# Performance work log

Hardware: AMD Instinct MI355X
Metric: run time of the kernel (lower is better)

## Reference

```python
import jax, jax.numpy as jnp
import numpy as np

N_NODES = 50000


def mean_aggregate(x, src, dst):
    # gather source features, scatter-sum to destinations, divide by in-degree
    msgs = x[src]                                             # [E, D]
    summed = jax.ops.segment_sum(msgs, dst, num_segments=N_NODES)  # [N, D]
    deg = jax.ops.segment_sum(jnp.ones_like(dst, dtype=x.dtype), dst,
                              num_segments=N_NODES)           # [N]
    return summed / jnp.clip(deg, 1.0)[:, None]


def sage_conv(x, src, dst, Wl, Wr, b):
    # PyG SAGEConv (aggr='mean'): lin_l(agg) + lin_r(x); bias only on lin_l
    agg = mean_aggregate(x, src, dst)
    return agg @ Wl + b + x @ Wr


def setup_inputs() -> dict:
    key = jax.random.key(0)
    ks = jax.random.split(key, 8)
    x = jax.random.normal(ks[0], (N_NODES, 64), dtype=jnp.float32)
    edge_index = jax.random.randint(ks[1], (2, 800000), 0, N_NODES, dtype=jnp.int32)
    W1l = jax.random.normal(ks[2], (64, 128), dtype=jnp.float32) * (1.0 / np.sqrt(64))
    W1r = jax.random.normal(ks[3], (64, 128), dtype=jnp.float32) * (1.0 / np.sqrt(64))
    b1 = jnp.zeros((128,), dtype=jnp.float32)
    W2l = jax.random.normal(ks[4], (128, 40), dtype=jnp.float32) * (1.0 / np.sqrt(128))
    W2r = jax.random.normal(ks[5], (128, 40), dtype=jnp.float32) * (1.0 / np.sqrt(128))
    b2 = jnp.zeros((40,), dtype=jnp.float32)
    return {"x": x, "edge_index": edge_index, "W1l": W1l, "W1r": W1r, "b1": b1,
            "W2l": W2l, "W2r": W2r, "b2": b2}


def reference(x, edge_index, W1l, W1r, b1, W2l, W2r, b2):
    src, dst = edge_index[0], edge_index[1]
    h = sage_conv(x, src, dst, W1l, W1r, b1)
    h = jax.nn.relu(h)
    # dropout p=0.5 is identity in eval mode (self.training=False)
    h = sage_conv(h, src, dst, W2l, W2r, b2)
    return h, jax.nn.log_softmax(h, axis=1)
```

## Files before the change

kernel.cpp:

```cpp
#include <hip/hip_runtime.h>
#include <hip/hip_bf16.h>
#include <math.h>

#define N_NODES 50000
#define N_EDGES 800000
#define D0 64
#define D1 128
#define D2 40

#define NB  256
#define NPB 196

typedef short s16x8 __attribute__((ext_vector_type(8)));
typedef float f32x4 __attribute__((ext_vector_type(4)));

static __device__ __forceinline__ unsigned short f2bf(float v) {
    __hip_bfloat16 hb = __float2bfloat16(v);
    return *(unsigned short*)&hb;
}

__global__ __launch_bounds__(256) void bucket_count_kernel(
        const int* __restrict__ dst, int* __restrict__ bcount, int E) {
    __shared__ int h[NB];
    int t = threadIdx.x;
    h[t] = 0;
    __syncthreads();
    int e0 = blockIdx.x * 2048;
    for (int i = t; i < 2048; i += 256) {
        int e = e0 + i;
        if (e < E) atomicAdd(&h[(unsigned)dst[e] / NPB], 1);
    }
    __syncthreads();
    if (h[t]) atomicAdd(&bcount[t], h[t]);
}

__global__ void bucket_scan_kernel(const int* __restrict__ bcount,
                                   int* __restrict__ bbase, int* __restrict__ bcursor) {
    __shared__ int sd[NB];
    int t = threadIdx.x;
    int v = bcount[t];
    sd[t] = v;
    __syncthreads();
    for (int off = 1; off < NB; off <<= 1) {
        int u = (t >= off) ? sd[t - off] : 0;
        __syncthreads();
        sd[t] += u;
        __syncthreads();
    }
    int ex = sd[t] - v;
    bbase[t] = ex;
    bcursor[t] = ex;
}

__global__ __launch_bounds__(256) void bucket_scatter_kernel(
        const int* __restrict__ src, const int* __restrict__ dst,
        int* __restrict__ bcursor, unsigned* __restrict__ ebuf, int E) {
    __shared__ int h[NB];
    __shared__ int base[NB];
    int t = threadIdx.x;
    int e0 = blockIdx.x * 4096;
    h[t] = 0;
    __syncthreads();
    for (int i = t; i < 4096; i += 256) {
        int e = e0 + i;
        if (e < E) atomicAdd(&h[(unsigned)dst[e] / NPB], 1);
    }
    __syncthreads();
    if (h[t] > 0) base[t] = atomicAdd(&bcursor[t], h[t]);
    h[t] = 0;
    __syncthreads();
    for (int i = t; i < 4096; i += 256) {
        int e = e0 + i;
        if (e < E) {
            unsigned d = (unsigned)dst[e];
            unsigned b = d / NPB;
            unsigned ld = d - b * NPB;
            int k = atomicAdd(&h[b], 1);
            ebuf[base[b] + k] = (ld << 17) | (unsigned)src[e];
        }
    }
}

__global__ __launch_bounds__(256) void bucket_fill_kernel(
        const unsigned* __restrict__ ebuf, const int* __restrict__ bbase,
        int* __restrict__ rowptr, int* __restrict__ csr, int E, int N) {
    __shared__ int cnt[256];
    __shared__ int sd[256];
    int b = blockIdx.x, t = threadIdx.x;
    int s0 = bbase[b];
    int s1 = (b < NB - 1) ? bbase[b + 1] : E;
    int lo = b * NPB;
    cnt[t] = 0;
    __syncthreads();
    for (int i = s0 + t; i < s1; i += 256)
        atomicAdd(&cnt[ebuf[i] >> 17], 1);
    __syncthreads();
    int v = cnt[t];
    sd[t] = v;
    __syncthreads();
    for (int off = 1; off < 256; off <<= 1) {
        int u = (t >= off) ? sd[t - off] : 0;
        __syncthreads();
        sd[t] += u;
        __syncthreads();
    }
    int ex = sd[t] - v;
    int node = lo + t;
    if (t < NPB && node < N) rowptr[node] = s0 + ex;
    cnt[t] = s0 + ex;
    __syncthreads();
    for (int i = s0 + t; i < s1; i += 256) {
        unsigned pk = ebuf[i];
        int p = atomicAdd(&cnt[pk >> 17], 1);
        csr[p] = (int)(pk & 0x1FFFFu);
    }
    if (b == NB - 1 && t == 0) rowptr[N] = E;
}


__global__ void cast_x_kernel(const float* __restrict__ x, unsigned short* __restrict__ xh, int n) {
    int i = (blockIdx.x * blockDim.x + threadIdx.x) * 4;
    if (i < n) {
        float4 v = *(const float4*)(x + i);
        xh[i + 0] = f2bf(v.x);
        xh[i + 1] = f2bf(v.y);
        xh[i + 2] = f2bf(v.z);
        xh[i + 3] = f2bf(v.w);
    }
}


__global__ void pack_w1_kernel(const float* __restrict__ W1l, const float* __restrict__ W1r,
                               unsigned short* __restrict__ Wpk) {
    int f = blockIdx.x;
    int lane = threadIdx.x;
    int nt = f & 7;
    int col = nt * 16 + (lane & 15);
    int kbase = (f >> 3) * 32 + (lane >> 4) * 8;
    unsigned short* o = Wpk + ((size_t)f * 64 + lane) * 8;
#pragma unroll
    for (int j = 0; j < 8; ++j) {
        int k = kbase + j;
        float w = (k < 64) ? W1r[k * 128 + col] : W1l[(k - 64) * 128 + col];
        o[j] = f2bf(w);
    }
}

__global__ void pack_w2_kernel(const float* __restrict__ W2l, const float* __restrict__ W2r,
                               unsigned short* __restrict__ Wpk) {
    int f = blockIdx.x;
    int lane = threadIdx.x;
    int nt = f % 5;
    int col = nt * 16 + (lane & 15);
    int kbase = (f / 5) * 32 + (lane >> 4) * 8;
    unsigned short* o = Wpk + ((size_t)f * 64 + lane) * 8;
#pragma unroll
    for (int j = 0; j < 8; ++j) {
        int k = kbase + j;
        float w = (col < 40) ? W2l[k * 40 + col] : W2r[k * 40 + (col - 40)];
        o[j] = f2bf(w);
    }
}


__global__ void agg1_kernel(const unsigned short* __restrict__ xh, const int* __restrict__ rowptr,
                            const int* __restrict__ csr, unsigned short* __restrict__ aggh, int N) {
    int wid = (blockIdx.x * blockDim.x + threadIdx.x) >> 6;
    int lane = threadIdx.x & 63;
    if (wid >= N) return;
    int beg = rowptr[wid], end = rowptr[wid + 1];
    int deg = end - beg;
    int l = lane & 7, g = lane >> 3;
    float acc[8];
#pragma unroll
    for (int k = 0; k < 8; ++k) acc[k] = 0.f;
    int jmax = (deg + 7) >> 3;
    for (int j = 0; j < jmax; j += 2) {
        int s[2]; float w[2];
#pragma unroll
        for (int u = 0; u < 2; ++u) {
            int slot = (j + u) * 8 + g;
            int e = beg + slot;
            e = (e < end) ? e : (end - 1);
            s[u] = csr[e];
            w[u] = (slot < deg) ? 1.f : 0.f;
        }
#pragma unroll
        for (int u = 0; u < 2; ++u) {
            uint4 v = *(const uint4*)(xh + (size_t)s[u] * D0 + l * 8);
            float f0 = __uint_as_float(v.x << 16), f1 = __uint_as_float(v.x & 0xffff0000u);
            float f2 = __uint_as_float(v.y << 16), f3 = __uint_as_float(v.y & 0xffff0000u);
            float f4 = __uint_as_float(v.z << 16), f5 = __uint_as_float(v.z & 0xffff0000u);
            float f6 = __uint_as_float(v.w << 16), f7 = __uint_as_float(v.w & 0xffff0000u);
            acc[0] = fmaf(w[u], f0, acc[0]); acc[1] = fmaf(w[u], f1, acc[1]);
            acc[2] = fmaf(w[u], f2, acc[2]); acc[3] = fmaf(w[u], f3, acc[3]);
            acc[4] = fmaf(w[u], f4, acc[4]); acc[5] = fmaf(w[u], f5, acc[5]);
            acc[6] = fmaf(w[u], f6, acc[6]); acc[7] = fmaf(w[u], f7, acc[7]);
        }
    }
#pragma unroll
    for (int off = 8; off <= 32; off <<= 1) {
#pragma unroll
        for (int k = 0; k < 8; ++k) acc[k] += __shfl_xor(acc[k], off);
    }
    float inv = 1.f / (float)max(deg, 1);
    if (g == 0) {
        unsigned o0 = (unsigned)f2bf(acc[0] * inv) | ((unsigned)f2bf(acc[1] * inv) << 16);
        unsigned o1 = (unsigned)f2bf(acc[2] * inv) | ((unsigned)f2bf(acc[3] * inv) << 16);
        unsigned o2 = (unsigned)f2bf(acc[4] * inv) | ((unsigned)f2bf(acc[5] * inv) << 16);
        unsigned o3 = (unsigned)f2bf(acc[6] * inv) | ((unsigned)f2bf(acc[7] * inv) << 16);
        uint4 pk; pk.x = o0; pk.y = o1; pk.z = o2; pk.w = o3;
        *(uint4*)(aggh + (size_t)wid * D0 + l * 8) = pk;
    }
}


__global__ void agg2_kernel(const float* __restrict__ p2, const float* __restrict__ r2,
                            const int* __restrict__ rowptr, const int* __restrict__ csr,
                            float* __restrict__ out, float* __restrict__ out2, int N) {
    int wid = (blockIdx.x * blockDim.x + threadIdx.x) >> 6;
    int lane = threadIdx.x & 63;
    if (wid >= N) return;
    int beg = rowptr[wid], end = rowptr[wid + 1];
    int deg = end - beg;
    int g = lane / 10;
    int l = lane - g * 10;
    bool gv = g < 6;
    float ax = 0.f, ay = 0.f, az = 0.f, aw = 0.f;
    int jmax = (deg + 5) / 6;
    for (int j = 0; j < jmax; j += 4) {
        int s[4]; float w[4];
#pragma unroll
        for (int u = 0; u < 4; ++u) {
            int slot = (j + u) * 6 + g;
            int e = beg + slot;
            e = (e < end) ? e : (end - 1);
            s[u] = csr[e];
            w[u] = (gv && slot < deg) ? 1.f : 0.f;
        }
#pragma unroll
        for (int u = 0; u < 4; ++u) {
            float4 v = *(const float4*)(p2 + (size_t)s[u] * D2 + l * 4);
            ax = fmaf(w[u], v.x, ax); ay = fmaf(w[u], v.y, ay);
            az = fmaf(w[u], v.z, az); aw = fmaf(w[u], v.w, aw);
        }
    }
    {
        float bx = __shfl(ax, lane + 30), by = __shfl(ay, lane + 30),
              bz = __shfl(az, lane + 30), bw = __shfl(aw, lane + 30);
        if (g < 3) { ax += bx; ay += by; az += bz; aw += bw; }
        bx = __shfl(ax, lane + 20); by = __shfl(ay, lane + 20);
        bz = __shfl(az, lane + 20); bw = __shfl(aw, lane + 20);
        if (g == 0) { ax += bx; ay += by; az += bz; aw += bw; }
        bx = __shfl(ax, lane + 10); by = __shfl(ay, lane + 10);
        bz = __shfl(az, lane + 10); bw = __shfl(aw, lane + 10);
        if (g == 0) { ax += bx; ay += by; az += bz; aw += bw; }
    }
    float inv = 1.f / (float)max(deg, 1);
    bool wr = (lane < 10);
    float4 h2;
    if (wr) {
        float4 rr = *(const float4*)(r2 + (size_t)wid * D2 + lane * 4);
        h2.x = rr.x + ax * inv; h2.y = rr.y + ay * inv;
        h2.z = rr.z + az * inv; h2.w = rr.w + aw * inv;
        *(float4*)(out + (size_t)wid * D2 + lane * 4) = h2;
    }
    float m = wr ? fmaxf(fmaxf(h2.x, h2.y), fmaxf(h2.z, h2.w)) : -INFINITY;
#pragma unroll
    for (int off = 1; off < 64; off <<= 1) m = fmaxf(m, __shfl_xor(m, off));
    float s = 0.f;
    if (wr) s = expf(h2.x - m) + expf(h2.y - m) + expf(h2.z - m) + expf(h2.w - m);
#pragma unroll
    for (int off = 1; off < 64; off <<= 1) s += __shfl_xor(s, off);
    if (wr) {
        float lg = m + logf(s);
        float4 o; o.x = h2.x - lg; o.y = h2.y - lg; o.z = h2.z - lg; o.w = h2.w - lg;
        *(float4*)(out2 + (size_t)wid * D2 + lane * 4) = o;
    }
}

__global__ __launch_bounds__(256) void gemm1_mfma(
        const unsigned short* __restrict__ xh, const unsigned short* __restrict__ aggh,
        const unsigned short* __restrict__ Wpk, const float* __restrict__ b1,
        unsigned short* __restrict__ h, int N) {
    __shared__ __align__(16) unsigned short As[128 * 136];
    int t = threadIdx.x;
    int r0 = blockIdx.x * 128;
    for (int i = t; i < 2048; i += 256) {
        int r = i >> 4, c = i & 15;
        int gr = r0 + r; gr = (gr < N) ? gr : (N - 1);
        uint4 v = (c < 8) ? ((const uint4*)(xh + (size_t)gr * 64))[c]
                          : ((const uint4*)(aggh + (size_t)gr * 64))[c - 8];
        *(uint4*)(As + r * 136 + c * 8) = v;
    }
    __syncthreads();
    int w = t >> 6, lane = t & 63;
    int l15 = lane & 15, q = lane >> 4;
    f32x4 zero = {0.f, 0.f, 0.f, 0.f};
    f32x4 acc[2][8];
#pragma unroll
    for (int rt = 0; rt < 2; ++rt)
#pragma unroll
        for (int nt = 0; nt < 8; ++nt) acc[rt][nt] = zero;
    const unsigned short* abase = As + (w * 32 + l15) * 136 + q * 8;
#pragma unroll
    for (int ks = 0; ks < 4; ++ks) {
        s16x8 a0 = *(const s16x8*)(abase + ks * 32);
        s16x8 a1 = *(const s16x8*)(abase + 16 * 136 + ks * 32);
        s16x8 b[8];
#pragma unroll
        for (int nt = 0; nt < 8; ++nt)
            b[nt] = *(const s16x8*)(Wpk + ((size_t)(ks * 8 + nt) * 64 + lane) * 8);
#pragma unroll
        for (int nt = 0; nt < 8; ++nt) {
            acc[0][nt] = __builtin_amdgcn_mfma_f32_16x16x32_bf16(a0, b[nt], acc[0][nt], 0, 0, 0);
            acc[1][nt] = __builtin_amdgcn_mfma_f32_16x16x32_bf16(a1, b[nt], acc[1][nt], 0, 0, 0);
        }
    }
    int rbase = r0 + w * 32 + q * 4;
#pragma unroll
    for (int nt = 0; nt < 8; ++nt) {
        int col = nt * 16 + l15;
        float bias = b1[col];
#pragma unroll
        for (int rt = 0; rt < 2; ++rt) {
#pragma unroll
            for (int reg = 0; reg < 4; ++reg) {
                int row = rbase + rt * 16 + reg;
                if (row < N)
                    h[(size_t)row * 128 + col] = f2bf(fmaxf(acc[rt][nt][reg] + bias, 0.f));
            }
        }
    }
}

__global__ __launch_bounds__(256) void gemm2_mfma(
        const unsigned short* __restrict__ hq, const unsigned short* __restrict__ Wpk,
        const float* __restrict__ b2,
        float* __restrict__ p2, float* __restrict__ r2, int N) {
    __shared__ __align__(16) unsigned short As[128 * 136];
    int t = threadIdx.x;
    int r0 = blockIdx.x * 128;
    for (int i = t; i < 2048; i += 256) {
        int r = i >> 4, c = i & 15;
        int gr = r0 + r; gr = (gr < N) ? gr : (N - 1);
        uint4 v = ((const uint4*)(hq + (size_t)gr * 128))[c];
        *(uint4*)(As + r * 136 + c * 8) = v;
    }
    __syncthreads();
    int w = t >> 6, lane = t & 63;
    int l15 = lane & 15, q = lane >> 4;
    f32x4 zero = {0.f, 0.f, 0.f, 0.f};
    f32x4 acc[2][5];
#pragma unroll
    for (int rt = 0; rt < 2; ++rt)
#pragma unroll
        for (int nt = 0; nt < 5; ++nt) acc[rt][nt] = zero;
    const unsigned short* abase = As + (w * 32 + l15) * 136 + q * 8;
#pragma unroll
    for (int ks = 0; ks < 4; ++ks) {
        s16x8 a0 = *(const s16x8*)(abase + ks * 32);
        s16x8 a1 = *(const s16x8*)(abase + 16 * 136 + ks * 32);
        s16x8 b[5];
#pragma unroll
        for (int nt = 0; nt < 5; ++nt)
            b[nt] = *(const s16x8*)(Wpk + ((size_t)(ks * 5 + nt) * 64 + lane) * 8);
#pragma unroll
        for (int nt = 0; nt < 5; ++nt) {
            acc[0][nt] = __builtin_amdgcn_mfma_f32_16x16x32_bf16(a0, b[nt], acc[0][nt], 0, 0, 0);
            acc[1][nt] = __builtin_amdgcn_mfma_f32_16x16x32_bf16(a1, b[nt], acc[1][nt], 0, 0, 0);
        }
    }
    int rbase = r0 + w * 32 + q * 4;
#pragma unroll
    for (int nt = 0; nt < 5; ++nt) {
        int col = nt * 16 + l15;
        bool isp = col < 40;
        int oc = isp ? col : (col - 40);
        float bias = isp ? 0.f : b2[oc];
#pragma unroll
        for (int rt = 0; rt < 2; ++rt) {
#pragma unroll
            for (int reg = 0; reg < 4; ++reg) {
                int row = rbase + rt * 16 + reg;
                if (row < N) {
                    float v = acc[rt][nt][reg] + bias;
                    if (isp) p2[(size_t)row * 40 + oc] = v;
                    else     r2[(size_t)row * 40 + oc] = v;
                }
            }
        }
    }
}


extern "C" void kernel_launch(void* const* d_in, const int* in_sizes, int n_in,
                              void* d_out, int out_size, void* d_ws, size_t ws_size,
                              hipStream_t stream) {
    const float* x   = (const float*)d_in[0];
    const int*   ei  = (const int*)d_in[1];
    const float* W1l = (const float*)d_in[2];
    const float* W1r = (const float*)d_in[3];
    const float* b1  = (const float*)d_in[4];
    const float* W2l = (const float*)d_in[5];
    const float* W2r = (const float*)d_in[6];
    const float* b2  = (const float*)d_in[7];
    float* out = (float*)d_out;

    const int N = N_NODES;
    const int E = in_sizes[1] / 2;
    const int* src = ei;
    const int* dst = ei + E;

    char* p = (char*)d_ws;
    auto alloc = [&](size_t bytes) -> void* {
        void* r = (void*)p;
        p += (bytes + 255) & ~(size_t)255;
        return r;
    };
    int*      rowptr  = (int*)alloc((size_t)(N + 1) * 4);
    int*      csr     = (int*)alloc((size_t)E * 4);
    unsigned* ebuf    = (unsigned*)alloc((size_t)E * 4);
    int*      bcount  = (int*)alloc(NB * 4);
    int*      bbase   = (int*)alloc(NB * 4);
    int*      bcursor = (int*)alloc(NB * 4);
    unsigned short* xh    = (unsigned short*)alloc((size_t)N * D0 * 2);
    unsigned short* aggh  = (unsigned short*)alloc((size_t)N * D0 * 2);
    unsigned short* hbuf  = (unsigned short*)alloc((size_t)N * D1 * 2);
    unsigned short* wpk1  = (unsigned short*)alloc((size_t)32 * 64 * 8 * 2);
    unsigned short* wpk2  = (unsigned short*)alloc((size_t)20 * 64 * 8 * 2);
    float* p2buf = (float*)alloc((size_t)N * D2 * 4);
    float* r2buf = (float*)alloc((size_t)N * D2 * 4);

    hipMemsetAsync(bcount, 0, NB * 4, stream);
    bucket_count_kernel<<<(E + 2047) / 2048, 256, 0, stream>>>(dst, bcount, E);
    bucket_scan_kernel<<<1, NB, 0, stream>>>(bcount, bbase, bcursor);
    bucket_scatter_kernel<<<(E + 4095) / 4096, 256, 0, stream>>>(src, dst, bcursor, ebuf, E);
    bucket_fill_kernel<<<NB, 256, 0, stream>>>(ebuf, bbase, rowptr, csr, E, N);

    cast_x_kernel<<<(N * D0 / 4 + 255) / 256, 256, 0, stream>>>(x, xh, N * D0);
    pack_w1_kernel<<<32, 64, 0, stream>>>(W1l, W1r, wpk1);
    pack_w2_kernel<<<20, 64, 0, stream>>>(W2l, W2r, wpk2);

    agg1_kernel<<<(N * 64 + 255) / 256, 256, 0, stream>>>(xh, rowptr, csr, aggh, N);
    gemm1_mfma<<<(N + 127) / 128, 256, 0, stream>>>(xh, aggh, wpk1, b1, hbuf, N);

    gemm2_mfma<<<(N + 127) / 128, 256, 0, stream>>>(hbuf, wpk2, b2, p2buf, r2buf, N);
    agg2_kernel<<<(N * 64 + 255) / 256, 256, 0, stream>>>(p2buf, r2buf, rowptr, csr,
                                                          out, out + (size_t)N * D2, N);
}
```

Measured before the change: 202.5 us.

## Fuse prep kernels into one launch and store layer-2 messages as bf16

Merges bucket counting, the x cast and both weight-packing kernels into a single prep kernel that branches on block index. Per-block histograms replace the global atomics and the memset, and the scan kernel now sums them. The layer-2 projected messages gathered by agg2 are stored in bf16 instead of fp32, halving gather traffic at some cost in precision. Together these cut launch count and memory traffic.

```diff
diff --git a/kernel.cpp b/kernel.cpp
--- a/kernel.cpp
+++ b/kernel.cpp
@@ -19,26 +19,70 @@
     return *(unsigned short*)&hb;
 }
 
-__global__ __launch_bounds__(256) void bucket_count_kernel(
-        const int* __restrict__ dst, int* __restrict__ bcount, int E) {
-    __shared__ int h[NB];
-    int t = threadIdx.x;
-    h[t] = 0;
-    __syncthreads();
-    int e0 = blockIdx.x * 2048;
-    for (int i = t; i < 2048; i += 256) {
-        int e = e0 + i;
-        if (e < E) atomicAdd(&h[(unsigned)dst[e] / NPB], 1);
-    }
-    __syncthreads();
-    if (h[t]) atomicAdd(&bcount[t], h[t]);
-}
-
-__global__ void bucket_scan_kernel(const int* __restrict__ bcount,
+__global__ __launch_bounds__(256) void prep_kernel(
+        const float* __restrict__ x, const int* __restrict__ dst,
+        const float* __restrict__ W1l, const float* __restrict__ W1r,
+        const float* __restrict__ W2l, const float* __restrict__ W2r,
+        unsigned short* __restrict__ xh, int* __restrict__ hist,
+        unsigned short* __restrict__ wpk1, unsigned short* __restrict__ wpk2,
+        int E, int nCount, int nCast) {
+    int b = blockIdx.x, t = threadIdx.x;
+    if (b < nCount) {
+        __shared__ int h[NB];
+        h[t] = 0;
+        __syncthreads();
+        int e0 = b * 2048;
+        for (int i = t; i < 2048; i += 256) {
+            int e = e0 + i;
+            if (e < E) atomicAdd(&h[(unsigned)dst[e] / NPB], 1);
+        }
+        __syncthreads();
+        hist[b * NB + t] = h[t];
+    } else if (b < nCount + nCast) {
+        int i = ((b - nCount) * 256 + t) * 4;
+        float4 v = *(const float4*)(x + i);
+        unsigned o0 = (unsigned)f2bf(v.x) | ((unsigned)f2bf(v.y) << 16);
+        unsigned o1 = (unsigned)f2bf(v.z) | ((unsigned)f2bf(v.w) << 16);
+        uint2 pk; pk.x = o0; pk.y = o1;
+        *(uint2*)(xh + i) = pk;
+    } else if (b < nCount + nCast + 8) {
+        int f = (b - nCount - nCast) * 4 + (t >> 6);
+        int lane = t & 63;
+        int nt = f & 7;
+        int col = nt * 16 + (lane & 15);
+        int kbase = (f >> 3) * 32 + (lane >> 4) * 8;
+        unsigned short* o = wpk1 + ((size_t)f * 64 + lane) * 8;
+#pragma unroll
+        for (int j = 0; j < 8; ++j) {
+            int k = kbase + j;
+            float w = (k < 64) ? W1r[k * 128 + col] : W1l[(k - 64) * 128 + col];
+            o[j] = f2bf(w);
+        }
+    } else {
+        int f = (b - nCount - nCast - 8) * 4 + (t >> 6);
+        if (f < 20) {
+            int lane = t & 63;
+            int nt = f % 5;
+            int col = nt * 16 + (lane & 15);
+            int kbase = (f / 5) * 32 + (lane >> 4) * 8;
+            unsigned short* o = wpk2 + ((size_t)f * 64 + lane) * 8;
+#pragma unroll
+            for (int j = 0; j < 8; ++j) {
+                int k = kbase + j;
+                float w = (col < 40) ? W2l[k * 40 + col] : W2r[k * 40 + (col - 40)];
+                o[j] = f2bf(w);
+            }
+        }
+    }
+}
+
+__global__ void bucket_scan_kernel(const int* __restrict__ hist, int nCount,
                                    int* __restrict__ bbase, int* __restrict__ bcursor) {
     __shared__ int sd[NB];
     int t = threadIdx.x;
-    int v = bcount[t];
+    int v = 0;
+#pragma unroll 4
+    for (int b = 0; b < nCount; ++b) v += hist[b * NB + t];
     sd[t] = v;
     __syncthreads();
     for (int off = 1; off < NB; off <<= 1) {
@@ -118,51 +162,6 @@
 }
 
 
-__global__ void cast_x_kernel(const float* __restrict__ x, unsigned short* __restrict__ xh, int n) {
-    int i = (blockIdx.x * blockDim.x + threadIdx.x) * 4;
-    if (i < n) {
-        float4 v = *(const float4*)(x + i);
-        xh[i + 0] = f2bf(v.x);
-        xh[i + 1] = f2bf(v.y);
-        xh[i + 2] = f2bf(v.z);
-        xh[i + 3] = f2bf(v.w);
-    }
-}
-
-
-__global__ void pack_w1_kernel(const float* __restrict__ W1l, const float* __restrict__ W1r,
-                               unsigned short* __restrict__ Wpk) {
-    int f = blockIdx.x;
-    int lane = threadIdx.x;
-    int nt = f & 7;
-    int col = nt * 16 + (lane & 15);
-    int kbase = (f >> 3) * 32 + (lane >> 4) * 8;
-    unsigned short* o = Wpk + ((size_t)f * 64 + lane) * 8;
-#pragma unroll
-    for (int j = 0; j < 8; ++j) {
-        int k = kbase + j;
-        float w = (k < 64) ? W1r[k * 128 + col] : W1l[(k - 64) * 128 + col];
-        o[j] = f2bf(w);
-    }
-}
-
-__global__ void pack_w2_kernel(const float* __restrict__ W2l, const float* __restrict__ W2r,
-                               unsigned short* __restrict__ Wpk) {
-    int f = blockIdx.x;
-    int lane = threadIdx.x;
-    int nt = f % 5;
-    int col = nt * 16 + (lane & 15);
-    int kbase = (f / 5) * 32 + (lane >> 4) * 8;
-    unsigned short* o = Wpk + ((size_t)f * 64 + lane) * 8;
-#pragma unroll
-    for (int j = 0; j < 8; ++j) {
-        int k = kbase + j;
-        float w = (col < 40) ? W2l[k * 40 + col] : W2r[k * 40 + (col - 40)];
-        o[j] = f2bf(w);
-    }
-}
-
-
 __global__ void agg1_kernel(const unsigned short* __restrict__ xh, const int* __restrict__ rowptr,
                             const int* __restrict__ csr, unsigned short* __restrict__ aggh, int N) {
     int wid = (blockIdx.x * blockDim.x + threadIdx.x) >> 6;
@@ -215,7 +214,7 @@
 }
 
 
-__global__ void agg2_kernel(const float* __restrict__ p2, const float* __restrict__ r2,
+__global__ void agg2_kernel(const unsigned short* __restrict__ p2h, const float* __restrict__ r2,
                             const int* __restrict__ rowptr, const int* __restrict__ csr,
                             float* __restrict__ out, float* __restrict__ out2, int N) {
     int wid = (blockIdx.x * blockDim.x + threadIdx.x) >> 6;
@@ -240,9 +239,11 @@
         }
 #pragma unroll
         for (int u = 0; u < 4; ++u) {
-            float4 v = *(const float4*)(p2 + (size_t)s[u] * D2 + l * 4);
-            ax = fmaf(w[u], v.x, ax); ay = fmaf(w[u], v.y, ay);
-            az = fmaf(w[u], v.z, az); aw = fmaf(w[u], v.w, aw);
+            uint2 v = *(const uint2*)(p2h + (size_t)s[u] * D2 + l * 4);
+            float f0 = __uint_as_float(v.x << 16), f1 = __uint_as_float(v.x & 0xffff0000u);
+            float f2 = __uint_as_float(v.y << 16), f3 = __uint_as_float(v.y & 0xffff0000u);
+            ax = fmaf(w[u], f0, ax); ay = fmaf(w[u], f1, ay);
+            az = fmaf(w[u], f2, az); aw = fmaf(w[u], f3, aw);
         }
     }
     {
@@ -337,7 +338,7 @@
 __global__ __launch_bounds__(256) void gemm2_mfma(
         const unsigned short* __restrict__ hq, const unsigned short* __restrict__ Wpk,
         const float* __restrict__ b2,
-        float* __restrict__ p2, float* __restrict__ r2, int N) {
+        unsigned short* __restrict__ p2h, float* __restrict__ r2, int N) {
     __shared__ __align__(16) unsigned short As[128 * 136];
     int t = threadIdx.x;
     int r0 = blockIdx.x * 128;
@@ -385,7 +386,7 @@
                 int row = rbase + rt * 16 + reg;
                 if (row < N) {
                     float v = acc[rt][nt][reg] + bias;
-                    if (isp) p2[(size_t)row * 40 + oc] = v;
+                    if (isp) p2h[(size_t)row * 40 + oc] = f2bf(v);
                     else     r2[(size_t)row * 40 + oc] = v;
                 }
             }
@@ -418,10 +419,13 @@
         p += (bytes + 255) & ~(size_t)255;
         return r;
     };
+    const int nCount = (E + 2047) / 2048;
+    const int nCast  = (N * D0) / 1024;
+
     int*      rowptr  = (int*)alloc((size_t)(N + 1) * 4);
     int*      csr     = (int*)alloc((size_t)E * 4);
     unsigned* ebuf    = (unsigned*)alloc((size_t)E * 4);
-    int*      bcount  = (int*)alloc(NB * 4);
+    int*      hist    = (int*)alloc((size_t)nCount * NB * 4);
     int*      bbase   = (int*)alloc(NB * 4);
     int*      bcursor = (int*)alloc(NB * 4);
     unsigned short* xh    = (unsigned short*)alloc((size_t)N * D0 * 2);
@@ -429,23 +433,19 @@
     unsigned short* hbuf  = (unsigned short*)alloc((size_t)N * D1 * 2);
     unsigned short* wpk1  = (unsigned short*)alloc((size_t)32 * 64 * 8 * 2);
     unsigned short* wpk2  = (unsigned short*)alloc((size_t)20 * 64 * 8 * 2);
-    float* p2buf = (float*)alloc((size_t)N * D2 * 4);
+    unsigned short* p2h   = (unsigned short*)alloc((size_t)N * D2 * 2);
     float* r2buf = (float*)alloc((size_t)N * D2 * 4);
 
-    hipMemsetAsync(bcount, 0, NB * 4, stream);
-    bucket_count_kernel<<<(E + 2047) / 2048, 256, 0, stream>>>(dst, bcount, E);
-    bucket_scan_kernel<<<1, NB, 0, stream>>>(bcount, bbase, bcursor);
+    prep_kernel<<<nCount + nCast + 8 + 5, 256, 0, stream>>>(
+        x, dst, W1l, W1r, W2l, W2r, xh, hist, wpk1, wpk2, E, nCount, nCast);
+    bucket_scan_kernel<<<1, NB, 0, stream>>>(hist, nCount, bbase, bcursor);
     bucket_scatter_kernel<<<(E + 4095) / 4096, 256, 0, stream>>>(src, dst, bcursor, ebuf, E);
     bucket_fill_kernel<<<NB, 256, 0, stream>>>(ebuf, bbase, rowptr, csr, E, N);
 
-    cast_x_kernel<<<(N * D0 / 4 + 255) / 256, 256, 0, stream>>>(x, xh, N * D0);
-    pack_w1_kernel<<<32, 64, 0, stream>>>(W1l, W1r, wpk1);
-    pack_w2_kernel<<<20, 64, 0, stream>>>(W2l, W2r, wpk2);
-
     agg1_kernel<<<(N * 64 + 255) / 256, 256, 0, stream>>>(xh, rowptr, csr, aggh, N);
     gemm1_mfma<<<(N + 127) / 128, 256, 0, stream>>>(xh, aggh, wpk1, b1, hbuf, N);
 
-    gemm2_mfma<<<(N + 127) / 128, 256, 0, stream>>>(hbuf, wpk2, b2, p2buf, r2buf, N);
-    agg2_kernel<<<(N * 64 + 255) / 256, 256, 0, stream>>>(p2buf, r2buf, rowptr, csr,
+    gemm2_mfma<<<(N + 127) / 128, 256, 0, stream>>>(hbuf, wpk2, b2, p2h, r2buf, N);
+    agg2_kernel<<<(N * 64 + 255) / 256, 256, 0, stream>>>(p2h, r2buf, rowptr, csr,
                                                           out, out + (size_t)N * D2, N);
 }
```

Result: no change. 203.6 us (+0.5%).
